# Performance work log

Measured on AMD Instinct MI355X. Metric: run time of the kernel, lower is better.

The kernel has to match this reference:

```python
import jax, jax.numpy as jnp
import numpy as np

D_MODEL = 1024
NHEAD = 16
HEAD_DIM = D_MODEL // NHEAD
B, S = 4, 2048
LN_EPS = 1e-5


def setup_inputs() -> dict:
    key = jax.random.key(0)
    ks = jax.random.split(key, 16)
    def lin(k, fin, fout):
        # torch nn.Linear default init scale ~ 1/sqrt(fin)
        s = 1.0 / np.sqrt(fin)
        kw, kb = jax.random.split(k)
        W = jax.random.uniform(kw, (fin, fout), jnp.float32, -s, s)
        b = jax.random.uniform(kb, (fout,), jnp.float32, -s, s)
        return W, b
    Wq, bq = lin(ks[0], D_MODEL, D_MODEL)
    Wk, bk = lin(ks[1], D_MODEL, D_MODEL)
    Wv, bv = lin(ks[2], D_MODEL, D_MODEL)
    Wo, bo = lin(ks[3], D_MODEL, D_MODEL)
    W1, b1 = lin(ks[4], D_MODEL, 2 * D_MODEL)
    W2, b2 = lin(ks[5], 2 * D_MODEL, D_MODEL)
    return {
        "query": jax.random.normal(ks[6], (B, S, D_MODEL), jnp.float32),
        "key": jax.random.normal(ks[7], (B, S, D_MODEL), jnp.float32),
        "value": jax.random.normal(ks[8], (B, S, D_MODEL), jnp.float32),
        "mask": jnp.ones((1, 1, S, S), dtype=bool),
        "Wq": Wq, "bq": bq, "Wk": Wk, "bk": bk, "Wv": Wv, "bv": bv,
        "Wo": Wo, "bo": bo,
        "ln_g": jnp.ones((D_MODEL,), jnp.float32),
        "ln_b": jnp.zeros((D_MODEL,), jnp.float32),
        "W1": W1, "b1": b1, "W2": W2, "b2": b2,
    }


def _layer_norm(x, g, b):
    mu = jnp.mean(x, axis=-1, keepdims=True)
    var = jnp.mean(jnp.square(x - mu), axis=-1, keepdims=True)
    return (x - mu) * jax.lax.rsqrt(var + LN_EPS) * g + b


def reference(query, key, value, mask, Wq, bq, Wk, bk, Wv, bv, Wo, bo,
              ln_g, ln_b, W1, b1, W2, b2):
    Bq, Sq, _ = query.shape
    # projections -> [B, H, S, hd]
    def split_heads(x):
        return x.reshape(Bq, -1, NHEAD, HEAD_DIM).transpose(0, 2, 1, 3)
    q = split_heads(query @ Wq + bq)
    k = split_heads(key @ Wk + bk)
    v = split_heads(value @ Wv + bv)
    scores = jnp.einsum("bhqd,bhkd->bhqk", q, k) / jnp.sqrt(
        jnp.asarray(HEAD_DIM, q.dtype))
    scores = jnp.where(mask, scores, jnp.asarray(-jnp.inf, scores.dtype))
    probs = jax.nn.softmax(scores, axis=-1)  # dropout is identity at eval
    ctx = jnp.einsum("bhqk,bhkd->bhqd", probs, v)
    ctx = ctx.transpose(0, 2, 1, 3).reshape(Bq, Sq, D_MODEL)
    out = ctx @ Wo + bo
    # residual with (pre-projection) query input, then layer norm
    out = _layer_norm(query + out, ln_g, ln_b)
    # FFN: Linear -> ReLU -> Linear
    out = jax.nn.relu(out @ W1 + b1) @ W2 + b2
    return out
```

## Files before the change

kernel.cpp:

```cpp
#include <hip/hip_runtime.h>

typedef unsigned short u16;
typedef u16 u16x4 __attribute__((ext_vector_type(4)));
typedef u16 u16x8 __attribute__((ext_vector_type(8)));
typedef __bf16 bf16x8 __attribute__((ext_vector_type(8)));
typedef float f32x4 __attribute__((ext_vector_type(4)));

__device__ __forceinline__ u16 f2bf(float f) {
  return __builtin_bit_cast(u16, (__bf16)f);
}

__device__ __forceinline__ bf16x8 ldbf8(const u16* p) {
  union { u16x8 u; bf16x8 b; } t;
  t.u = *(const u16x8*)p;
  return t.b;
}

__device__ __forceinline__ bf16x8 cat44(u16x4 a, u16x4 b) {
  union { u16x4 h[2]; bf16x8 v; } t;
  t.h[0] = a; t.h[1] = b;
  return t.v;
}

#if __has_builtin(__builtin_amdgcn_exp2f)
#define EXP2(x) __builtin_amdgcn_exp2f(x)
#else
#define EXP2(x) exp2f(x)
#endif

__device__ __forceinline__ void gl16(const u16* g, u16* l) {
  __builtin_amdgcn_global_load_lds(
      (const __attribute__((address_space(1))) void*)g,
      (__attribute__((address_space(3))) void*)l, 16, 0, 0);
}

struct PrepDesc { const float* W; u16* WT; int K; int N; };
struct Prep { PrepDesc d[6]; const float* cs[3]; u16* cd[3]; };

__global__ __launch_bounds__(256, 4) void prep_k(Prep p) {
  const int z = blockIdx.z;
  if (z < 6) {
    PrepDesc dd = p.d[z];
    const int n0 = blockIdx.x * 32, k0 = blockIdx.y * 32;
    if (n0 >= dd.N || k0 >= dd.K) return;
    __shared__ float tt[32][33];
    const int tx = threadIdx.x & 31, ty = threadIdx.x >> 5;
#pragma unroll
    for (int i = 0; i < 4; i++) {
      int k = ty + i * 8;
      tt[k][tx] = dd.W[(size_t)(k0 + k) * dd.N + n0 + tx];
    }
    __syncthreads();
#pragma unroll
    for (int i = 0; i < 4; i++) {
      int n = ty + i * 8;
      dd.WT[(size_t)(n0 + n) * dd.K + k0 + tx] = f2bf(tt[tx][n]);
    }
  } else {
    const float* src = p.cs[z - 6];
    u16* dst = p.cd[z - 6];
    size_t base = ((size_t)(blockIdx.y * 64 + blockIdx.x)) * 2048 + threadIdx.x * 4;
#pragma unroll
    for (int j = 0; j < 2; j++) {
      f32x4 v = *(const f32x4*)(src + base + j * 1024);
      u16x4 o;
      o.x = f2bf(v.x); o.y = f2bf(v.y); o.z = f2bf(v.z); o.w = f2bf(v.w);
      *(u16x4*)(dst + base + j * 1024) = o;
    }
  }
}

struct Acc44 { f32x4 a[4][4]; };

__device__ __forceinline__ void gemm_core(const u16* __restrict__ A,
                                          const u16* __restrict__ B,
                                          int m0, int n0, int K,
                                          int tid, int wm, int wn, int c, int quad,
                                          u16* sA, u16* sB, Acc44& acc) {
#pragma unroll
  for (int mi = 0; mi < 4; mi++)
#pragma unroll
    for (int ni = 0; ni < 4; ni++) acc.a[mi][ni] = 0.f;

  const int lane = tid & 63, w = tid >> 6;
  const int rsub = lane >> 3;
  const int c8 = (lane & 7) * 8;

  const u16* Ab = A + (size_t)m0 * K;
  const u16* Bb = B + (size_t)n0 * K;

  const int kIters = K >> 6;
  for (int kt = 0; kt < kIters; kt++) {
    const u16* Ag = Ab + kt * 64;
    const u16* Bg = Bb + kt * 64;
#pragma unroll
    for (int j = 0; j < 4; j++) {
      const int chunk = w * 4 + j;
      const int row = chunk * 8 + rsub;
      gl16(Ag + (size_t)row * K + c8, sA + chunk * 512);
      gl16(Bg + (size_t)row * K + c8, sB + chunk * 512);
    }
    __syncthreads();
#pragma unroll
    for (int ks = 0; ks < 2; ks++) {
      bf16x8 af[4], bg[4];
#pragma unroll
      for (int mi = 0; mi < 4; mi++)
        af[mi] = ldbf8(&sA[(wm + mi * 16 + c) * 64 + ks * 32 + quad * 8]);
#pragma unroll
      for (int ni = 0; ni < 4; ni++)
        bg[ni] = ldbf8(&sB[(wn + ni * 16 + c) * 64 + ks * 32 + quad * 8]);
#pragma unroll
      for (int mi = 0; mi < 4; mi++)
#pragma unroll
        for (int ni = 0; ni < 4; ni++)
          acc.a[mi][ni] = __builtin_amdgcn_mfma_f32_16x16x32_bf16(af[mi], bg[ni], acc.a[mi][ni], 0, 0, 0);
    }
    __syncthreads();
  }
}

__global__ __launch_bounds__(256, 3) void qkv_k(const u16* __restrict__ qb,
                                                const u16* __restrict__ kb,
                                                const u16* __restrict__ vb,
                                                const u16* __restrict__ WqT,
                                                const u16* __restrict__ WkT,
                                                const u16* __restrict__ WvT,
                                                const float* __restrict__ bq,
                                                const float* __restrict__ bk,
                                                const float* __restrict__ bv,
                                                u16* __restrict__ qp,
                                                u16* __restrict__ kp,
                                                u16* __restrict__ vp) {
  const int tid = threadIdx.x;
  const int lane = tid & 63, w = tid >> 6;
  const int c = lane & 15, quad = lane >> 4;
  const int z = blockIdx.z, bx = blockIdx.x, by = blockIdx.y;
  int n0, m0;
  const u16 *A, *B;
  if (z < 2) {
    n0 = (bx & 7) * 128; m0 = (by * 8 + (bx >> 3)) * 128;
    A = z ? kb : qb; B = z ? WkT : WqT;
  } else {
    n0 = bx * 128; m0 = by * 128;
    A = WvT; B = vb;
  }
  const int wm = (w >> 1) * 64, wn = (w & 1) * 64;

  __shared__ __attribute__((aligned(16))) u16 sA[128 * 64];
  __shared__ __attribute__((aligned(16))) u16 sB[128 * 64];
  Acc44 acc;
  gemm_core(A, B, m0, n0, 1024, tid, wm, wn, c, quad, sA, sB, acc);

#pragma unroll
  for (int mi = 0; mi < 4; mi++)
#pragma unroll
    for (int ni = 0; ni < 4; ni++)
#pragma unroll
      for (int r = 0; r < 4; r++) {
        int row = m0 + wm + mi * 16 + quad * 4 + r;
        int col = n0 + wn + ni * 16 + c;
        if (z < 2) {
          const float* bias = z ? bk : bq;
          u16* out = z ? kp : qp;
          float v = acc.a[mi][ni][r] + bias[col];
          int b = row >> 11, s = row & 2047, h = col >> 6, d = col & 63;
          out[(((size_t)(b * 16 + h) * 2048 + s) << 6) + d] = f2bf(v);
        } else {
          float v = acc.a[mi][ni][r] + bv[row];
          int b = col >> 11, s = col & 2047, h = row >> 6, d = row & 63;
          vp[(((size_t)(b * 16 + h) * 64 + d) << 11) + s] = f2bf(v);
        }
      }
}

template <int MODE>
__global__ __launch_bounds__(256, 3) void gemm128_k(const u16* __restrict__ A,
                                                    const u16* __restrict__ B,
                                                    const float* __restrict__ bias,
                                                    const float* __restrict__ resid,
                                                    void* __restrict__ Out,
                                                    int M, int N, int K) {
  const int tid = threadIdx.x;
  const int lane = tid & 63, w = tid >> 6;
  const int c = lane & 15, quad = lane >> 4;
  const int n0 = blockIdx.x * 128, m0 = blockIdx.y * 128;
  const int wm = (w >> 1) * 64, wn = (w & 1) * 64;

  __shared__ __attribute__((aligned(16))) u16 sA[128 * 64];
  __shared__ __attribute__((aligned(16))) u16 sB[128 * 64];
  Acc44 acc;
  gemm_core(A, B, m0, n0, K, tid, wm, wn, c, quad, sA, sB, acc);

#pragma unroll
  for (int mi = 0; mi < 4; mi++)
#pragma unroll
    for (int ni = 0; ni < 4; ni++)
#pragma unroll
      for (int r = 0; r < 4; r++) {
        int row = m0 + wm + mi * 16 + quad * 4 + r;
        int col = n0 + wn + ni * 16 + c;
        float v = acc.a[mi][ni][r] + bias[col];
        if constexpr (MODE == 1) {
          v += resid[(size_t)row * N + col];
          ((float*)Out)[(size_t)row * N + col] = v;
        } else if constexpr (MODE == 2) {
          v = fmaxf(v, 0.f);
          ((u16*)Out)[(size_t)row * N + col] = f2bf(v);
        } else {
          ((float*)Out)[(size_t)row * N + col] = v;
        }
      }
}

__global__ __launch_bounds__(256, 4) void attn_k(const u16* __restrict__ Qp,
                                                 const u16* __restrict__ Kp,
                                                 const u16* __restrict__ Vt,
                                                 u16* __restrict__ ctx) {
  const int tid = threadIdx.x, lane = tid & 63, w = tid >> 6;
  const int c = lane & 15, quad = lane >> 4;
  const int bh = blockIdx.x, qt = blockIdx.y;
  const int b = bh >> 4, h = bh & 15;

  __shared__ u16 lds[2 * 64 * 72];
  u16* Kt = lds;
  u16* Vs = lds + 64 * 72;

  const u16* Qb = Qp + ((size_t)bh * 2048 + qt * 128 + w * 32) * 64;
  bf16x8 aq[2][2];
#pragma unroll
  for (int st = 0; st < 2; st++)
#pragma unroll
    for (int ks = 0; ks < 2; ks++)
      aq[st][ks] = ldbf8(Qb + (st * 16 + c) * 64 + ks * 32 + quad * 8);

  const float SC = 0.18033688011112042f;
  f32x4 o[2][4];
  float rs[2] = {0.f, 0.f};
#pragma unroll
  for (int st = 0; st < 2; st++)
#pragma unroll
    for (int dt = 0; dt < 4; dt++) o[st][dt] = 0.f;

  const u16* Kb0 = Kp + (size_t)bh * 2048 * 64;
  const u16* Vb0 = Vt + (size_t)bh * 64 * 2048;
  const int sr = tid >> 3, sc8 = (tid & 7) * 8;

  u16x8 kr[2], vr[2];
#pragma unroll
  for (int j = 0; j < 2; j++) {
    kr[j] = *(const u16x8*)(Kb0 + ((size_t)(j * 32 + sr)) * 64 + sc8);
    vr[j] = *(const u16x8*)(Vb0 + (size_t)(j * 32 + sr) * 2048 + sc8);
  }

  for (int kt = 0; kt < 32; kt++) {
    __syncthreads();
#pragma unroll
    for (int j = 0; j < 2; j++) {
      *(u16x8*)&Kt[(j * 32 + sr) * 72 + sc8] = kr[j];
      *(u16x8*)&Vs[(j * 32 + sr) * 72 + sc8] = vr[j];
    }
    __syncthreads();
    if (kt < 31) {
#pragma unroll
      for (int j = 0; j < 2; j++) {
        kr[j] = *(const u16x8*)(Kb0 + ((size_t)(kt + 1) * 64 + j * 32 + sr) * 64 + sc8);
        vr[j] = *(const u16x8*)(Vb0 + (size_t)(j * 32 + sr) * 2048 + (kt + 1) * 64 + sc8);
      }
    }

    f32x4 sT[2][4];
#pragma unroll
    for (int ct = 0; ct < 4; ct++) {
      bf16x8 ka0 = ldbf8(&Kt[(ct * 16 + c) * 72 + 0 + quad * 8]);
      bf16x8 ka1 = ldbf8(&Kt[(ct * 16 + c) * 72 + 32 + quad * 8]);
#pragma unroll
      for (int st = 0; st < 2; st++) {
        f32x4 t = 0.f;
        t = __builtin_amdgcn_mfma_f32_16x16x32_bf16(ka0, aq[st][0], t, 0, 0, 0);
        t = __builtin_amdgcn_mfma_f32_16x16x32_bf16(ka1, aq[st][1], t, 0, 0, 0);
        sT[st][ct] = t;
      }
    }

    u16x4 pb[2][4];
#pragma unroll
    for (int st = 0; st < 2; st++)
#pragma unroll
      for (int ct = 0; ct < 4; ct++)
#pragma unroll
        for (int r = 0; r < 4; r++) {
          float pf = EXP2(sT[st][ct][r] * SC);
          rs[st] += pf;
          pb[st][ct][r] = f2bf(pf);
        }

#pragma unroll
    for (int kh = 0; kh < 2; kh++) {
      bf16x8 pB[2];
#pragma unroll
      for (int st = 0; st < 2; st++) pB[st] = cat44(pb[st][2 * kh], pb[st][2 * kh + 1]);
#pragma unroll
      for (int dt = 0; dt < 4; dt++) {
        const u16* vrow = &Vs[(dt * 16 + c) * 72 + kh * 32 + quad * 4];
        bf16x8 A8 = cat44(*(const u16x4*)vrow, *(const u16x4*)(vrow + 16));
#pragma unroll
        for (int st = 0; st < 2; st++)
          o[st][dt] = __builtin_amdgcn_mfma_f32_16x16x32_bf16(A8, pB[st], o[st][dt], 0, 0, 0);
      }
    }
  }

  float inv[2];
#pragma unroll
  for (int st = 0; st < 2; st++) {
    float r = rs[st];
    r += __shfl_xor(r, 16);
    r += __shfl_xor(r, 32);
    inv[st] = 1.0f / r;
  }

  __syncthreads();
  u16* Ob = lds + w * 2304;
#pragma unroll
  for (int st = 0; st < 2; st++)
#pragma unroll
    for (int dt = 0; dt < 4; dt++)
#pragma unroll
      for (int r = 0; r < 4; r++)
        Ob[(st * 16 + c) * 72 + dt * 16 + quad * 4 + r] = f2bf(o[st][dt][r] * inv[st]);
#pragma unroll
  for (int j = 0; j < 4; j++) {
    int r_ = j * 8 + (lane >> 3), dc = (lane & 7) * 8;
    u16x8 v = *(const u16x8*)&Ob[r_ * 72 + dc];
    int s_ = qt * 128 + w * 32 + r_;
    *(u16x8*)&ctx[((size_t)b * 2048 + s_) * 1024 + h * 64 + dc] = v;
  }
}

__global__ __launch_bounds__(256, 4) void ln_k(const float* __restrict__ X,
                                               const float* __restrict__ g,
                                               const float* __restrict__ bt,
                                               u16* __restrict__ out) {
  const int row = blockIdx.x, tid = threadIdx.x;
  const float* x = X + (size_t)row * 1024;
  f32x4 v = *(const f32x4*)(x + tid * 4);
  float s = v.x + v.y + v.z + v.w;
  float sq = v.x * v.x + v.y * v.y + v.z * v.z + v.w * v.w;
#pragma unroll
  for (int off = 1; off < 64; off <<= 1) {
    s += __shfl_xor(s, off);
    sq += __shfl_xor(sq, off);
  }
  __shared__ float red[4][2];
  if ((tid & 63) == 0) { red[tid >> 6][0] = s; red[tid >> 6][1] = sq; }
  __syncthreads();
  s = red[0][0] + red[1][0] + red[2][0] + red[3][0];
  sq = red[0][1] + red[1][1] + red[2][1] + red[3][1];
  float mu = s * (1.0f / 1024.0f);
  float var = sq * (1.0f / 1024.0f) - mu * mu;
  float rstd = rsqrtf(var + 1e-5f);
#pragma unroll
  for (int j = 0; j < 4; j++) {
    int col = tid * 4 + j;
    out[(size_t)row * 1024 + col] = f2bf((v[j] - mu) * rstd * g[col] + bt[col]);
  }
}

extern "C" void kernel_launch(void* const* d_in, const int* in_sizes, int n_in,
                              void* d_out, int out_size, void* d_ws, size_t ws_size,
                              hipStream_t stream) {
  const float* query = (const float*)d_in[0];
  const float* key_  = (const float*)d_in[1];
  const float* value = (const float*)d_in[2];
  const float* Wq = (const float*)d_in[4];  const float* bq = (const float*)d_in[5];
  const float* Wk = (const float*)d_in[6];  const float* bk = (const float*)d_in[7];
  const float* Wv = (const float*)d_in[8];  const float* bv = (const float*)d_in[9];
  const float* Wo = (const float*)d_in[10]; const float* bo = (const float*)d_in[11];
  const float* ln_g = (const float*)d_in[12]; const float* ln_b = (const float*)d_in[13];
  const float* W1 = (const float*)d_in[14]; const float* b1 = (const float*)d_in[15];
  const float* W2 = (const float*)d_in[16]; const float* b2 = (const float*)d_in[17];

  const size_t MB = 1u << 20;
  if (ws_size < 112 * MB) return;
  char* ws = (char*)d_ws;
  u16* WqT = (u16*)(ws + 0 * MB);
  u16* WkT = (u16*)(ws + 2 * MB);
  u16* WvT = (u16*)(ws + 4 * MB);
  u16* WoT = (u16*)(ws + 6 * MB);
  u16* W1T = (u16*)(ws + 8 * MB);
  u16* W2T = (u16*)(ws + 12 * MB);
  u16* qb  = (u16*)(ws + 16 * MB);
  u16* kb  = (u16*)(ws + 32 * MB);
  u16* vb  = (u16*)(ws + 48 * MB);
  u16* qp  = (u16*)(ws + 64 * MB);
  u16* kp  = (u16*)(ws + 80 * MB);
  u16* vp  = (u16*)(ws + 96 * MB);
  u16* ctxp = (u16*)(ws + 16 * MB);
  float* resid = (float*)(ws + 32 * MB);
  u16* xb = (u16*)(ws + 64 * MB);
  u16* hb = (u16*)(ws + 80 * MB);

  Prep p;
  p.d[0] = {Wq, WqT, 1024, 1024}; p.d[1] = {Wk, WkT, 1024, 1024};
  p.d[2] = {Wv, WvT, 1024, 1024}; p.d[3] = {Wo, WoT, 1024, 1024};
  p.d[4] = {W1, W1T, 1024, 2048}; p.d[5] = {W2, W2T, 2048, 1024};
  p.cs[0] = query; p.cs[1] = key_; p.cs[2] = value;
  p.cd[0] = qb;    p.cd[1] = kb;   p.cd[2] = vb;
  prep_k<<<dim3(64, 64, 9), 256, 0, stream>>>(p);

  qkv_k<<<dim3(64, 8, 3), 256, 0, stream>>>(qb, kb, vb, WqT, WkT, WvT,
                                            bq, bk, bv, qp, kp, vp);

  attn_k<<<dim3(64, 16), 256, 0, stream>>>(qp, kp, vp, ctxp);

  gemm128_k<1><<<dim3(8, 64), 256, 0, stream>>>(ctxp, WoT, bo, query, resid, 8192, 1024, 1024);

  ln_k<<<8192, 256, 0, stream>>>(resid, ln_g, ln_b, xb);

  gemm128_k<2><<<dim3(16, 64), 256, 0, stream>>>(xb, W1T, b1, nullptr, hb, 8192, 2048, 1024);
  gemm128_k<3><<<dim3(8, 64), 256, 0, stream>>>(hb, W2T, b2, nullptr, (float*)d_out, 8192, 1024, 2048);
}
```

Measured before the change: 492.8 us.

## Double-buffer GEMMs with 256x128 tiles, swizzled LDS, and 8-wave ping-pong scheduling

Replaces the single-buffered 128x128 GEMM core with a 256x128 tile run by 512 threads. The loop double-buffers LDS and issues next-tile global-to-LDS loads between MFMA phases, using s_setprio and barriers to interleave waves. LDS rows are XOR-swizzled to cut bank conflicts. Workgroup IDs are remapped so neighbouring blocks land on the same XCD for L2 reuse. The cost is more LDS per block (96KB) and fewer, larger workgroups, which may reduce occupancy and leave tail imbalance on the smaller grids.

New measurement: 521.6 us. 5.9% more time.

```diff
diff --git a/kernel.cpp b/kernel.cpp
--- a/kernel.cpp
+++ b/kernel.cpp
@@ -27,6 +27,8 @@
 #else
 #define EXP2(x) exp2f(x)
 #endif
+
+#define MFMA16(a, b, c) __builtin_amdgcn_mfma_f32_16x16x32_bf16(a, b, c, 0, 0, 0)
 
 __device__ __forceinline__ void gl16(const u16* g, u16* l) {
   __builtin_amdgcn_global_load_lds(
@@ -72,55 +74,119 @@
 
 struct Acc44 { f32x4 a[4][4]; };
 
-__device__ __forceinline__ void gemm_core(const u16* __restrict__ A,
-                                          const u16* __restrict__ B,
-                                          int m0, int n0, int K,
-                                          int tid, int wm, int wn, int c, int quad,
-                                          u16* sA, u16* sB, Acc44& acc) {
+__device__ __forceinline__ void stage_unit(const u16* src, u16* dst, int K,
+                                           int w, int rsub, int c8x) {
+#pragma unroll
+  for (int j = 0; j < 2; j++) {
+    const int chunk = w * 2 + j;
+    const int row = chunk * 8 + rsub;
+    gl16(src + (size_t)row * K + c8x, dst + chunk * 512);
+  }
+}
+
+__device__ __forceinline__ void gemm_core256(const u16* __restrict__ A,
+                                             const u16* __restrict__ B,
+                                             int m0, int n0, int K,
+                                             int tid, u16* ldsA, u16* ldsB,
+                                             Acc44& acc) {
 #pragma unroll
   for (int mi = 0; mi < 4; mi++)
 #pragma unroll
     for (int ni = 0; ni < 4; ni++) acc.a[mi][ni] = 0.f;
 
   const int lane = tid & 63, w = tid >> 6;
+  const int c = lane & 15, quad = lane >> 4;
   const int rsub = lane >> 3;
-  const int c8 = (lane & 7) * 8;
+  const int c8x = ((lane & 7) ^ rsub) * 8;
+  const int s0 = (quad ^ (c & 7)) * 8;
+  const int s1 = ((4 + quad) ^ (c & 7)) * 8;
+  const int wm = (w >> 1) * 64, wn = (w & 1) * 64;
 
   const u16* Ab = A + (size_t)m0 * K;
   const u16* Bb = B + (size_t)n0 * K;
 
-  const int kIters = K >> 6;
-  for (int kt = 0; kt < kIters; kt++) {
-    const u16* Ag = Ab + kt * 64;
-    const u16* Bg = Bb + kt * 64;
-#pragma unroll
-    for (int j = 0; j < 4; j++) {
-      const int chunk = w * 4 + j;
-      const int row = chunk * 8 + rsub;
-      gl16(Ag + (size_t)row * K + c8, sA + chunk * 512);
-      gl16(Bg + (size_t)row * K + c8, sB + chunk * 512);
-    }
-    __syncthreads();
-#pragma unroll
-    for (int ks = 0; ks < 2; ks++) {
-      bf16x8 af[4], bg[4];
-#pragma unroll
-      for (int mi = 0; mi < 4; mi++)
-        af[mi] = ldbf8(&sA[(wm + mi * 16 + c) * 64 + ks * 32 + quad * 8]);
+  const int NT = K >> 6;
+  stage_unit(Ab, ldsA, K, w, rsub, c8x);
+  stage_unit(Ab + (size_t)128 * K, ldsA + 8192, K, w, rsub, c8x);
+  stage_unit(Bb, ldsB, K, w, rsub, c8x);
+
+  for (int t = 0; t < NT; t++) {
+    const int cur = t & 1, nxt = cur ^ 1;
+    const u16* A_c = ldsA + cur * 16384;
+    const u16* B_c = ldsB + cur * 8192;
+    u16* A_n = ldsA + nxt * 16384;
+    u16* B_n = ldsB + nxt * 8192;
+    const u16* Ag = Ab + (t + 1) * 64;
+    const u16* Bg = Bb + (t + 1) * 64;
+    const bool hn = (t + 1 < NT);
+
+    bf16x8 bg[4], af[2];
+
+    if (hn) {
+      stage_unit(Ag, A_n, K, w, rsub, c8x);
+      asm volatile("s_waitcnt vmcnt(2)" ::: "memory");
+    } else {
+      asm volatile("s_waitcnt vmcnt(0)" ::: "memory");
+    }
+    __builtin_amdgcn_s_barrier();
+#pragma unroll
+    for (int ni = 0; ni < 4; ni++)
+      bg[ni] = ldbf8(&B_c[(wn + ni * 16 + c) * 64 + s0]);
+    af[0] = ldbf8(&A_c[(wm + 0 * 16 + c) * 64 + s0]);
+    af[1] = ldbf8(&A_c[(wm + 1 * 16 + c) * 64 + s0]);
+    __builtin_amdgcn_s_setprio(1);
+#pragma unroll
+    for (int mi = 0; mi < 2; mi++)
 #pragma unroll
       for (int ni = 0; ni < 4; ni++)
-        bg[ni] = ldbf8(&sB[(wn + ni * 16 + c) * 64 + ks * 32 + quad * 8]);
-#pragma unroll
-      for (int mi = 0; mi < 4; mi++)
-#pragma unroll
-        for (int ni = 0; ni < 4; ni++)
-          acc.a[mi][ni] = __builtin_amdgcn_mfma_f32_16x16x32_bf16(af[mi], bg[ni], acc.a[mi][ni], 0, 0, 0);
-    }
-    __syncthreads();
-  }
-}
-
-__global__ __launch_bounds__(256, 3) void qkv_k(const u16* __restrict__ qb,
+        acc.a[mi][ni] = MFMA16(af[mi], bg[ni], acc.a[mi][ni]);
+    __builtin_amdgcn_s_setprio(0);
+    __builtin_amdgcn_s_barrier();
+
+    af[0] = ldbf8(&A_c[(wm + 2 * 16 + c) * 64 + s0]);
+    af[1] = ldbf8(&A_c[(wm + 3 * 16 + c) * 64 + s0]);
+    if (hn) stage_unit(Ag + (size_t)128 * K, A_n + 8192, K, w, rsub, c8x);
+    __builtin_amdgcn_s_barrier();
+    __builtin_amdgcn_s_setprio(1);
+#pragma unroll
+    for (int mi = 0; mi < 2; mi++)
+#pragma unroll
+      for (int ni = 0; ni < 4; ni++)
+        acc.a[2 + mi][ni] = MFMA16(af[mi], bg[ni], acc.a[2 + mi][ni]);
+    __builtin_amdgcn_s_setprio(0);
+    __builtin_amdgcn_s_barrier();
+
+#pragma unroll
+    for (int ni = 0; ni < 4; ni++)
+      bg[ni] = ldbf8(&B_c[(wn + ni * 16 + c) * 64 + s1]);
+    af[0] = ldbf8(&A_c[(wm + 0 * 16 + c) * 64 + s1]);
+    af[1] = ldbf8(&A_c[(wm + 1 * 16 + c) * 64 + s1]);
+    if (hn) stage_unit(Bg, B_n, K, w, rsub, c8x);
+    __builtin_amdgcn_s_barrier();
+    __builtin_amdgcn_s_setprio(1);
+#pragma unroll
+    for (int mi = 0; mi < 2; mi++)
+#pragma unroll
+      for (int ni = 0; ni < 4; ni++)
+        acc.a[mi][ni] = MFMA16(af[mi], bg[ni], acc.a[mi][ni]);
+    __builtin_amdgcn_s_setprio(0);
+    __builtin_amdgcn_s_barrier();
+
+    af[0] = ldbf8(&A_c[(wm + 2 * 16 + c) * 64 + s1]);
+    af[1] = ldbf8(&A_c[(wm + 3 * 16 + c) * 64 + s1]);
+    __builtin_amdgcn_s_barrier();
+    __builtin_amdgcn_s_setprio(1);
+#pragma unroll
+    for (int mi = 0; mi < 2; mi++)
+#pragma unroll
+      for (int ni = 0; ni < 4; ni++)
+        acc.a[2 + mi][ni] = MFMA16(af[mi], bg[ni], acc.a[2 + mi][ni]);
+    __builtin_amdgcn_s_setprio(0);
+    __builtin_amdgcn_s_barrier();
+  }
+}
+
+__global__ __launch_bounds__(512, 2) void qkv_k(const u16* __restrict__ qb,
                                                 const u16* __restrict__ kb,
                                                 const u16* __restrict__ vb,
                                                 const u16* __restrict__ WqT,
@@ -135,22 +201,22 @@
   const int tid = threadIdx.x;
   const int lane = tid & 63, w = tid >> 6;
   const int c = lane & 15, quad = lane >> 4;
-  const int z = blockIdx.z, bx = blockIdx.x, by = blockIdx.y;
-  int n0, m0;
+  const int z = blockIdx.y;
+  int f = blockIdx.x;
+  f = (f & 7) * 32 + (f >> 3);
+  int bx, by;
+  if (z < 2) { bx = f & 7;  by = f >> 3; }
+  else       { bx = f & 63; by = f >> 6; }
+  const int n0 = bx * 128, m0 = by * 256;
   const u16 *A, *B;
-  if (z < 2) {
-    n0 = (bx & 7) * 128; m0 = (by * 8 + (bx >> 3)) * 128;
-    A = z ? kb : qb; B = z ? WkT : WqT;
-  } else {
-    n0 = bx * 128; m0 = by * 128;
-    A = WvT; B = vb;
-  }
+  if (z < 2) { A = z ? kb : qb; B = z ? WkT : WqT; }
+  else       { A = WvT; B = vb; }
   const int wm = (w >> 1) * 64, wn = (w & 1) * 64;
 
-  __shared__ __attribute__((aligned(16))) u16 sA[128 * 64];
-  __shared__ __attribute__((aligned(16))) u16 sB[128 * 64];
+  __shared__ __attribute__((aligned(16))) u16 ldsA[2 * 16384];
+  __shared__ __attribute__((aligned(16))) u16 ldsB[2 * 8192];
   Acc44 acc;
-  gemm_core(A, B, m0, n0, 1024, tid, wm, wn, c, quad, sA, sB, acc);
+  gemm_core256(A, B, m0, n0, 1024, tid, ldsA, ldsB, acc);
 
 #pragma unroll
   for (int mi = 0; mi < 4; mi++)
@@ -175,22 +241,27 @@
 }
 
 template <int MODE>
-__global__ __launch_bounds__(256, 3) void gemm128_k(const u16* __restrict__ A,
-                                                    const u16* __restrict__ B,
-                                                    const float* __restrict__ bias,
-                                                    const float* __restrict__ resid,
-                                                    void* __restrict__ Out,
-                                                    int M, int N, int K) {
+__global__ __launch_bounds__(512, 2) void gemm_k(const u16* __restrict__ A,
+                                                 const u16* __restrict__ B,
+                                                 const float* __restrict__ bias,
+                                                 const float* __restrict__ resid,
+                                                 void* __restrict__ Out,
+                                                 int M, int N, int K) {
   const int tid = threadIdx.x;
   const int lane = tid & 63, w = tid >> 6;
   const int c = lane & 15, quad = lane >> 4;
-  const int n0 = blockIdx.x * 128, m0 = blockIdx.y * 128;
+  const int nx = gridDim.x;
+  const int nwg = nx * gridDim.y;
+  int f = blockIdx.x + nx * blockIdx.y;
+  f = (f & 7) * (nwg >> 3) + (f >> 3);
+  const int bx = f % nx, by = f / nx;
+  const int n0 = bx * 128, m0 = by * 256;
   const int wm = (w >> 1) * 64, wn = (w & 1) * 64;
 
-  __shared__ __attribute__((aligned(16))) u16 sA[128 * 64];
-  __shared__ __attribute__((aligned(16))) u16 sB[128 * 64];
+  __shared__ __attribute__((aligned(16))) u16 ldsA[2 * 16384];
+  __shared__ __attribute__((aligned(16))) u16 ldsB[2 * 8192];
   Acc44 acc;
-  gemm_core(A, B, m0, n0, K, tid, wm, wn, c, quad, sA, sB, acc);
+  gemm_core256(A, B, m0, n0, K, tid, ldsA, ldsB, acc);
 
 #pragma unroll
   for (int mi = 0; mi < 4; mi++)
@@ -409,15 +480,15 @@
   p.cd[0] = qb;    p.cd[1] = kb;   p.cd[2] = vb;
   prep_k<<<dim3(64, 64, 9), 256, 0, stream>>>(p);
 
-  qkv_k<<<dim3(64, 8, 3), 256, 0, stream>>>(qb, kb, vb, WqT, WkT, WvT,
-                                            bq, bk, bv, qp, kp, vp);
+  qkv_k<<<dim3(256, 3), 512, 0, stream>>>(qb, kb, vb, WqT, WkT, WvT,
+                                          bq, bk, bv, qp, kp, vp);
 
   attn_k<<<dim3(64, 16), 256, 0, stream>>>(qp, kp, vp, ctxp);
 
-  gemm128_k<1><<<dim3(8, 64), 256, 0, stream>>>(ctxp, WoT, bo, query, resid, 8192, 1024, 1024);
+  gemm_k<1><<<dim3(8, 32), 512, 0, stream>>>(ctxp, WoT, bo, query, resid, 8192, 1024, 1024);
 
   ln_k<<<8192, 256, 0, stream>>>(resid, ln_g, ln_b, xb);
 
-  gemm128_k<2><<<dim3(16, 64), 256, 0, stream>>>(xb, W1T, b1, nullptr, hb, 8192, 2048, 1024);
-  gemm128_k<3><<<dim3(8, 64), 256, 0, stream>>>(hb, W2T, b2, nullptr, (float*)d_out, 8192, 1024, 2048);
-}
+  gemm_k<2><<<dim3(16, 32), 512, 0, stream>>>(xb, W1T, b1, nullptr, hb, 8192, 2048, 1024);
+  gemm_k<3><<<dim3(8, 32), 512, 0, stream>>>(hb, W2T, b2, nullptr, (float*)d_out, 8192, 1024, 2048);
+}
```
